# Kernel tuning notes

Hardware: AMD Instinct MI355X
Metric: run time of the kernel (lower is better)

## Reference

```python
import jax, jax.numpy as jnp
import numpy as np
from collections import defaultdict

H = 24; W = 24          # patch grid
B0 = 64                 # original batch (len(batch_id))
B = 128                 # total batch incl. augmented copies
C_IN = 256; HID = 128; HEADS_S = 2; OUT = 256; K = 9; NCLS = 8


def _build_space_edges():
    # knn_graph on the normalized meshgrid coords; identical for every image -> offset copies.
    P = H * W
    coords = np.stack(np.meshgrid(np.arange(H), np.arange(W), indexing='ij'), -1).reshape(-1, 2).astype(np.float32)
    cn = coords / coords.max()
    d = ((cn[:, None, :] - cn[None, :, :]) ** 2).sum(-1)
    np.fill_diagonal(d, np.inf)              # loop=False
    nbr = np.argsort(d, axis=1)[:, :K]       # [P, K] neighbor (source) ids
    off = (np.arange(B0) * P)[:, None, None]
    src = (nbr[None] + off).reshape(-1)
    dst = (np.broadcast_to(np.arange(P)[:, None], (P, K))[None] + off).reshape(-1)
    return np.stack([src, dst]).astype(np.int64)


def _build_view_edges(bid_all):
    groups = defaultdict(list)
    for i, c in enumerate(bid_all.tolist()):
        groups[c].append(i)
    ei = []
    for c, mem in groups.items():
        for a in range(len(mem)):
            for b in range(a + 1, len(mem)):
                i, j = mem[a], mem[b]
                if i >= B0 and j >= B0:
                    continue               # skip augmented-augmented pairs
                ei.append((i, j)); ei.append((j, i))
    return np.array(ei, dtype=np.int64).T


def setup_inputs() -> dict:
    key = jax.random.key(0)
    ks = jax.random.split(key, 8)
    bid = np.repeat(np.arange(NCLS), B0 // NCLS).astype(np.int64)
    bid_all = np.concatenate([bid, bid])
    s = 0.05
    return {
        'x': jax.random.normal(ks[0], (B, C_IN, H, W), jnp.float32),
        'batch_id_all': jnp.asarray(bid_all),
        'batch_id': jnp.asarray(bid),
        'edge_index_space': jnp.asarray(_build_space_edges()),
        'edge_index_view': jnp.asarray(_build_view_edges(bid_all)),
        'W_space': jax.random.normal(ks[1], (C_IN, HEADS_S * HID), jnp.float32) * s,
        'att_src_space': jax.random.normal(ks[2], (HEADS_S, HID), jnp.float32) * s,
        'att_dst_space': jax.random.normal(ks[3], (HEADS_S, HID), jnp.float32) * s,
        'bias_space': jnp.zeros((HEADS_S * HID,), jnp.float32),
        'W_view': jax.random.normal(ks[4], (HEADS_S * HID, OUT), jnp.float32) * s,
        'att_src_view': jax.random.normal(ks[5], (1, OUT), jnp.float32) * s,
        'att_dst_view': jax.random.normal(ks[6], (1, OUT), jnp.float32) * s,
        'bias_view': jnp.zeros((OUT,), jnp.float32),
    }


def _gat(xn, edges, Wm, a_src, a_dst, bias, heads, outc):
    # PyG GATConv: linear -> per-edge leaky_relu attn -> segment softmax over dst -> scatter-add
    N = xn.shape[0]
    loops = jnp.arange(N, dtype=edges.dtype)              # add_self_loops=True
    src = jnp.concatenate([edges[0], loops])
    dst = jnp.concatenate([edges[1], loops])
    h = (xn @ Wm).reshape(N, heads, outc)                 # [N, H, C]
    a_s = jnp.sum(h * a_src[None], -1)                    # [N, H]
    a_d = jnp.sum(h * a_dst[None], -1)
    e = jax.nn.leaky_relu(a_s[src] + a_d[dst], 0.2)       # [E, H]
    m = jax.ops.segment_max(e, dst, num_segments=N)
    ee = jnp.exp(e - m[dst])
    ssum = jax.ops.segment_sum(ee, dst, num_segments=N)
    alpha = ee / (ssum[dst] + 1e-16)
    out = jax.ops.segment_sum(h[src] * alpha[..., None], dst, num_segments=N)
    return out.reshape(N, heads * outc) + bias            # concat=True


def reference(x, batch_id_all, batch_id, edge_index_space, edge_index_view,
              W_space, att_src_space, att_dst_space, bias_space,
              W_view, att_src_view, att_dst_view, bias_view):
    P = H * W
    node = x[:B0].transpose(0, 2, 3, 1).reshape(-1, C_IN)                # [B0*P, C_in]
    x_space = _gat(node, edge_index_space, W_space, att_src_space,
                   att_dst_space, bias_space, HEADS_S, HID)              # [B0*P, 256]
    emb = x_space.reshape(B0, P, -1).mean(axis=1)                        # per-image mean pool
    emb_all = emb[jnp.arange(B) % B0]                                    # augmented i -> i % B0
    feat = _gat(emb_all, edge_index_view, W_view, att_src_view,
                att_dst_view, bias_view, 1, OUT)                         # [B, 256]
    C = feat.shape[1]
    x_view = 0.5 * x_space.reshape(B0, P, C) + 0.5 * feat[:B0][:, None, :]
    # torch does .reshape(-1, C).view(B, C, H, W): a raw row-major reinterpret
    return x_view.reshape(B0, C, H, W)
```

## Files before the change

kernel.cpp:

```cpp
#include <hip/hip_runtime.h>

#define PGRID 576
#define NB0   64
#define NBTOT 128
#define CIN   256
#define KNN   9
#define NNODE (NB0 * PGRID)

typedef __attribute__((ext_vector_type(8))) short short8;
typedef __attribute__((ext_vector_type(4))) float f32x4;

__device__ __forceinline__ float bf2f(unsigned short u) {
    union { unsigned int i; float f; } v; v.i = ((unsigned int)u) << 16; return v.f;
}
__device__ __forceinline__ unsigned short f2b(float f) {
    unsigned int u = __float_as_uint(f);
    return (unsigned short)((u + 0x7FFFu + ((u >> 16) & 1u)) >> 16);
}

__global__ __launch_bounds__(256) void prep_w(const float* __restrict__ W,
                                              unsigned short* __restrict__ Wt) {
    __shared__ float tile[64][65];
    const int c0 = blockIdx.x * 64, j0 = blockIdx.y * 64;
    const int t = threadIdx.x, lo = t % 64, hi = t / 64;
#pragma unroll
    for (int r = 0; r < 16; ++r)
        tile[r * 4 + hi][lo] = W[(size_t)(c0 + r * 4 + hi) * 256 + j0 + lo];
    __syncthreads();
#pragma unroll
    for (int r = 0; r < 16; ++r)
        Wt[(size_t)(j0 + r * 4 + hi) * 256 + c0 + lo] = f2b(tile[lo][r * 4 + hi]);
}

__global__ __launch_bounds__(256) void prep_x(const float* __restrict__ x,
                                              unsigned short* __restrict__ xbf) {
    __shared__ float tile[64][65];
    const int pt = blockIdx.x, ct = blockIdx.y, b = blockIdx.z;
    const int t = threadIdx.x, lo = t % 64, hi = t / 64;
    const float* xb = x + (size_t)b * CIN * PGRID;
#pragma unroll
    for (int r = 0; r < 16; ++r)
        tile[r * 4 + hi][lo] = xb[(size_t)(ct * 64 + r * 4 + hi) * PGRID + pt * 64 + lo];
    __syncthreads();
    const size_t nbase = (size_t)b * PGRID + pt * 64;
#pragma unroll
    for (int r = 0; r < 16; ++r)
        xbf[(nbase + r * 4 + hi) * 256 + ct * 64 + lo] = f2b(tile[lo][r * 4 + hi]);
}

__global__ __launch_bounds__(256) void gemm_mfma(const unsigned short* __restrict__ xbf,
                                                 const unsigned short* __restrict__ Wt,
                                                 unsigned short* __restrict__ h) {
    __shared__ char lds[65536];
    const int t  = threadIdx.x;
    const int n0 = blockIdx.x * 64;
    const int j0 = blockIdx.y * 64;
    const char* Ab = (const char*)xbf + (size_t)n0 * 512;
    const char* Bb = (const char*)Wt  + (size_t)j0 * 512;

#pragma unroll
    for (int pass = 0; pass < 8; ++pass) {
        const int p    = pass * 4096 + t * 16;
        const int row  = p >> 9;
        const int k16  = (p >> 4) & 31;
        const int src  = k16 ^ (row & 7);
        char* ldA = lds + pass * 4096 + (t & 192) * 16;
        char* ldB = ldA + 32768;
        __builtin_amdgcn_global_load_lds(Ab + (size_t)row * 512 + src * 16, ldA, 16, 0, 0);
        __builtin_amdgcn_global_load_lds(Bb + (size_t)row * 512 + src * 16, ldB, 16, 0, 0);
    }
    __syncthreads();

    const int l  = t & 63, w = t >> 6;
    const int qb = l >> 4;
    const int r7 = l & 7;
    const int rowA = w * 16 + (l & 15);
    const char* lA = lds + rowA * 512;
    f32x4 acc[4] = {};
#pragma unroll
    for (int ks = 0; ks < 8; ++ks) {
        const int q = (ks << 2) + qb;
        short8 a = *(const short8*)(lA + ((q ^ r7) << 4));
#pragma unroll
        for (int f = 0; f < 4; ++f) {
            short8 b = *(const short8*)(lds + 32768 + (f * 16 + (l & 15)) * 512 + ((q ^ r7) << 4));
            acc[f] = __builtin_amdgcn_mfma_f32_16x16x32_bf16(a, b, acc[f], 0, 0, 0);
        }
    }
    const int nb = n0 + w * 16 + ((l >> 4) << 2);
    const int jb = j0 + (l & 15);
#pragma unroll
    for (int f = 0; f < 4; ++f)
#pragma unroll
        for (int r = 0; r < 4; ++r)
            h[(size_t)(nb + r) * 256 + jb + f * 16] = f2b(acc[f][r]);
}

__global__ __launch_bounds__(256) void att_scores(const unsigned short* __restrict__ h,
                                                  const float* __restrict__ att_src,
                                                  const float* __restrict__ att_dst,
                                                  float* __restrict__ as_,
                                                  float* __restrict__ ad_) {
    const int wave = threadIdx.x >> 6;
    const int lane = threadIdx.x & 63;
    const int n = blockIdx.x * 4 + wave;
    const unsigned short* hr = h + (size_t)n * 256;
    float h0 = bf2f(hr[lane]), h1 = bf2f(hr[lane + 64]);
    float h2 = bf2f(hr[lane + 128]), h3 = bf2f(hr[lane + 192]);
    float s0 = h0 * att_src[lane]       + h1 * att_src[lane + 64];
    float s1 = h2 * att_src[lane + 128] + h3 * att_src[lane + 192];
    float d0 = h0 * att_dst[lane]       + h1 * att_dst[lane + 64];
    float d1 = h2 * att_dst[lane + 128] + h3 * att_dst[lane + 192];
#pragma unroll
    for (int off = 32; off > 0; off >>= 1) {
        s0 += __shfl_down(s0, off);
        s1 += __shfl_down(s1, off);
        d0 += __shfl_down(d0, off);
        d1 += __shfl_down(d1, off);
    }
    if (lane == 0) {
        as_[n * 2] = s0; as_[n * 2 + 1] = s1;
        ad_[n * 2] = d0; ad_[n * 2 + 1] = d1;
    }
}

__global__ __launch_bounds__(256) void space_gather(const unsigned short* __restrict__ h,
                                                    const float* __restrict__ as_,
                                                    const float* __restrict__ ad_,
                                                    const int* __restrict__ esrc,
                                                    const float* __restrict__ bias,
                                                    float* __restrict__ xs) {
    __shared__ int   s_src[10];
    __shared__ float s_e[10][2];
    const int n = blockIdx.x;
    const int t = threadIdx.x;
    if (t < 10) {
        int src = (t < 9) ? esrc[(size_t)n * KNN + t] : n;
        s_src[t] = src;
        float ad0 = ad_[n * 2], ad1 = ad_[n * 2 + 1];
        float e0 = as_[src * 2]     + ad0;
        float e1 = as_[src * 2 + 1] + ad1;
        s_e[t][0] = e0 >= 0.f ? e0 : 0.2f * e0;
        s_e[t][1] = e1 >= 0.f ? e1 : 0.2f * e1;
    }
    __syncthreads();
    const int head = t >> 7;
    float m = -1e30f;
#pragma unroll
    for (int k = 0; k < 10; ++k) m = fmaxf(m, s_e[k][head]);
    float wt[10];
    float ssum = 0.f;
#pragma unroll
    for (int k = 0; k < 10; ++k) { wt[k] = __expf(s_e[k][head] - m); ssum += wt[k]; }
    const float inv = 1.f / (ssum + 1e-16f);
    float out = 0.f;
#pragma unroll
    for (int k = 0; k < 10; ++k) out += wt[k] * bf2f(h[(size_t)s_src[k] * 256 + t]);
    xs[(size_t)n * 256 + t] = out * inv + bias[t];
}

__global__ __launch_bounds__(256) void pool_partial(const float* __restrict__ xs,
                                                    float* __restrict__ emb) {
    const int b = blockIdx.x, ch = blockIdx.y, j = threadIdx.x;
    const float* base = xs + ((size_t)b * PGRID + ch * 64) * 256 + j;
    float s = 0.f;
#pragma unroll 8
    for (int p = 0; p < 64; ++p) s += base[p * 256];
    atomicAdd(&emb[b * 256 + j], s);
}

__global__ __launch_bounds__(256) void view_linear(const float* __restrict__ emb,
                                                   const float* __restrict__ Wv,
                                                   const float* __restrict__ att_s,
                                                   const float* __restrict__ att_d,
                                                   float* __restrict__ hv,
                                                   float* __restrict__ asv,
                                                   float* __restrict__ adv) {
    __shared__ float er[256];
    __shared__ float red[2][256];
    const int i = blockIdx.x;
    const int j = threadIdx.x;
    er[j] = emb[(i % 64) * 256 + j] * (1.f / 576.f);
    __syncthreads();
    float acc = 0.f;
    for (int c = 0; c < 256; ++c) acc += er[c] * Wv[c * 256 + j];
    hv[(size_t)i * 256 + j] = acc;
    red[0][j] = acc * att_s[j];
    red[1][j] = acc * att_d[j];
    __syncthreads();
    for (int off = 128; off > 0; off >>= 1) {
        if (j < off) { red[0][j] += red[0][j + off]; red[1][j] += red[1][j + off]; }
        __syncthreads();
    }
    if (j == 0) { asv[i] = red[0][0]; adv[i] = red[1][0]; }
}

__global__ __launch_bounds__(256) void view_gather(const float* __restrict__ hv,
                                                   const float* __restrict__ asv,
                                                   const float* __restrict__ adv,
                                                   const int* __restrict__ ev,
                                                   int Ev,
                                                   const float* __restrict__ bias,
                                                   float* __restrict__ feat) {
    __shared__ int cnt;
    __shared__ int s_src[32];
    const int d = blockIdx.x;
    const int t = threadIdx.x;
    if (t == 0) cnt = 0;
    __syncthreads();
    for (int e = t; e < Ev; e += 256) {
        if (ev[Ev + e] == d) {
            int pos = atomicAdd(&cnt, 1);
            s_src[pos] = ev[e];
        }
    }
    __syncthreads();
    const int ns = cnt;
    const float adval = adv[d];
    float m = -1e30f;
    float ev_[16];
#pragma unroll 1
    for (int k = 0; k < ns; ++k) {
        float e = asv[s_src[k]] + adval;
        e = e >= 0.f ? e : 0.2f * e;
        ev_[k] = e;
        m = fmaxf(m, e);
    }
    float eself = asv[d] + adval;
    eself = eself >= 0.f ? eself : 0.2f * eself;
    m = fmaxf(m, eself);
    float ssum = 0.f;
#pragma unroll 1
    for (int k = 0; k < ns; ++k) { ev_[k] = __expf(ev_[k] - m); ssum += ev_[k]; }
    float wself = __expf(eself - m);
    ssum += wself;
    const float inv = 1.f / (ssum + 1e-16f);
    float out = 0.f;
#pragma unroll 1
    for (int k = 0; k < ns; ++k) out += ev_[k] * hv[(size_t)s_src[k] * 256 + t];
    out += wself * hv[(size_t)d * 256 + t];
    feat[d * 256 + t] = out * inv + bias[t];
}

__global__ __launch_bounds__(256) void combine(const float* __restrict__ xs,
                                               const float* __restrict__ feat,
                                               float* __restrict__ out, int ntot4) {
    int i = blockIdx.x * blockDim.x + threadIdx.x;
    if (i >= ntot4) return;
    size_t f = (size_t)i * 4;
    int b = (int)(f / (PGRID * 256));
    int j = (int)(f & 255);
    float4 a  = *(const float4*)(xs + f);
    float4 fb = *(const float4*)(feat + b * 256 + j);
    float4 o;
    o.x = 0.5f * (a.x + fb.x);
    o.y = 0.5f * (a.y + fb.y);
    o.z = 0.5f * (a.z + fb.z);
    o.w = 0.5f * (a.w + fb.w);
    *(float4*)(out + f) = o;
}

extern "C" void kernel_launch(void* const* d_in, const int* in_sizes, int n_in,
                              void* d_out, int out_size, void* d_ws, size_t ws_size,
                              hipStream_t stream) {
    const float* x        = (const float*)d_in[0];
    const int*   e_space  = (const int*)d_in[3];
    const int*   e_view   = (const int*)d_in[4];
    const float* W_space  = (const float*)d_in[5];
    const float* att_ss   = (const float*)d_in[6];
    const float* att_ds   = (const float*)d_in[7];
    const float* bias_s   = (const float*)d_in[8];
    const float* W_view   = (const float*)d_in[9];
    const float* att_sv   = (const float*)d_in[10];
    const float* att_dv   = (const float*)d_in[11];
    const float* bias_v   = (const float*)d_in[12];
    float* out = (float*)d_out;

    const int Ev = in_sizes[4] / 2;

    char* ws = (char*)d_ws;
    unsigned short* hbf = (unsigned short*)ws;
    unsigned short* xbf = (unsigned short*)(ws + 18874368);
    unsigned short* Wt  = (unsigned short*)(ws + 2 * 18874368);
    float* xs   = (float*)(ws + 2 * 18874368 + 131072);
    float* as_  = xs  + (size_t)NNODE * 256;
    float* ad_  = as_ + NNODE * 2;
    float* emb  = ad_ + NNODE * 2;
    float* hv   = emb + 64 * 256;
    float* asv  = hv  + 128 * 256;
    float* adv  = asv + 128;
    float* feat = adv + 128;

    prep_w<<<dim3(4, 4), 256, 0, stream>>>(W_space, Wt);
    prep_x<<<dim3(9, 4, 64), 256, 0, stream>>>(x, xbf);
    gemm_mfma<<<dim3(NNODE / 64, 4), 256, 0, stream>>>(xbf, Wt, hbf);
    att_scores<<<NNODE / 4, 256, 0, stream>>>(hbf, att_ss, att_ds, as_, ad_);
    space_gather<<<NNODE, 256, 0, stream>>>(hbf, as_, ad_, e_space, bias_s, xs);
    hipMemsetAsync(emb, 0, 64 * 256 * sizeof(float), stream);
    pool_partial<<<dim3(64, 9), 256, 0, stream>>>(xs, emb);
    view_linear<<<NBTOT, 256, 0, stream>>>(emb, W_view, att_sv, att_dv, hv, asv, adv);
    view_gather<<<NB0, 256, 0, stream>>>(hv, asv, adv, e_view, Ev, bias_v, feat);

    const int ntot4 = NB0 * PGRID * 256 / 4;
    combine<<<(ntot4 + 255) / 256, 256, 0, stream>>>(xs, feat, out, ntot4);
}
```

Before: 242.2 us.

## Fuse x transpose/convert and attention scores into a full-width MFMA GEMM

Removes the separate prep_x transpose pass and att_scores kernel. The GEMM now reads fp32 x directly in its channel-major layout, converts it to bf16 in registers, and computes all 256 output columns per block, so each wave computes attention dot products from its accumulators. The gather handles two nodes per block with vectorized bf16x2 loads. Pooling writes per-segment partial sums instead of using atomics and a memset. The cost is strided, uncoalesced global reads of x and a much larger register footprint (64 floats plus 16 accumulators), which may lower occupancy.

New measurement: 216.7 us. -10.5%, faster.

```diff
diff --git a/kernel.cpp b/kernel.cpp
--- a/kernel.cpp
+++ b/kernel.cpp
@@ -2,7 +2,6 @@
 
 #define PGRID 576
 #define NB0   64
-#define NBTOT 128
 #define CIN   256
 #define KNN   9
 #define NNODE (NB0 * PGRID)
@@ -32,144 +31,176 @@
         Wt[(size_t)(j0 + r * 4 + hi) * 256 + c0 + lo] = f2b(tile[lo][r * 4 + hi]);
 }
 
-__global__ __launch_bounds__(256) void prep_x(const float* __restrict__ x,
-                                              unsigned short* __restrict__ xbf) {
-    __shared__ float tile[64][65];
-    const int pt = blockIdx.x, ct = blockIdx.y, b = blockIdx.z;
-    const int t = threadIdx.x, lo = t % 64, hi = t / 64;
-    const float* xb = x + (size_t)b * CIN * PGRID;
-#pragma unroll
-    for (int r = 0; r < 16; ++r)
-        tile[r * 4 + hi][lo] = xb[(size_t)(ct * 64 + r * 4 + hi) * PGRID + pt * 64 + lo];
-    __syncthreads();
-    const size_t nbase = (size_t)b * PGRID + pt * 64;
-#pragma unroll
-    for (int r = 0; r < 16; ++r)
-        xbf[(nbase + r * 4 + hi) * 256 + ct * 64 + lo] = f2b(tile[lo][r * 4 + hi]);
-}
-
-__global__ __launch_bounds__(256) void gemm_mfma(const unsigned short* __restrict__ xbf,
-                                                 const unsigned short* __restrict__ Wt,
-                                                 unsigned short* __restrict__ h) {
-    __shared__ char lds[65536];
+__global__ __launch_bounds__(256) void gemm_fused(
+    const float* __restrict__ x, const unsigned short* __restrict__ Wt,
+    const float* __restrict__ att_src, const float* __restrict__ att_dst,
+    unsigned short* __restrict__ h, float* __restrict__ as_, float* __restrict__ ad_) {
+    __shared__ char ldsB[65536];
+    const int bx = blockIdx.x;
     const int t  = threadIdx.x;
-    const int n0 = blockIdx.x * 64;
-    const int j0 = blockIdx.y * 64;
-    const char* Ab = (const char*)xbf + (size_t)n0 * 512;
-    const char* Bb = (const char*)Wt  + (size_t)j0 * 512;
-
-#pragma unroll
-    for (int pass = 0; pass < 8; ++pass) {
-        const int p    = pass * 4096 + t * 16;
-        const int row  = p >> 9;
-        const int k16  = (p >> 4) & 31;
-        const int src  = k16 ^ (row & 7);
-        char* ldA = lds + pass * 4096 + (t & 192) * 16;
-        char* ldB = ldA + 32768;
-        __builtin_amdgcn_global_load_lds(Ab + (size_t)row * 512 + src * 16, ldA, 16, 0, 0);
-        __builtin_amdgcn_global_load_lds(Bb + (size_t)row * 512 + src * 16, ldB, 16, 0, 0);
-    }
-    __syncthreads();
-
-    const int l  = t & 63, w = t >> 6;
-    const int qb = l >> 4;
-    const int r7 = l & 7;
-    const int rowA = w * 16 + (l & 15);
-    const char* lA = lds + rowA * 512;
-    f32x4 acc[4] = {};
-#pragma unroll
-    for (int ks = 0; ks < 8; ++ks) {
-        const int q = (ks << 2) + qb;
-        short8 a = *(const short8*)(lA + ((q ^ r7) << 4));
-#pragma unroll
-        for (int f = 0; f < 4; ++f) {
-            short8 b = *(const short8*)(lds + 32768 + (f * 16 + (l & 15)) * 512 + ((q ^ r7) << 4));
-            acc[f] = __builtin_amdgcn_mfma_f32_16x16x32_bf16(a, b, acc[f], 0, 0, 0);
-        }
-    }
-    const int nb = n0 + w * 16 + ((l >> 4) << 2);
-    const int jb = j0 + (l & 15);
-#pragma unroll
-    for (int f = 0; f < 4; ++f)
+    const int b  = bx / 9;
+    const int p0 = (bx % 9) * 64;
+    const int n0 = bx * 64;
+    const int l = t & 63, w = t >> 6;
+    const int l4 = l >> 4, l15 = l & 15;
+    const float* xb = x + (size_t)b * (CIN * PGRID);
+
+    {
+        const int jrow = t >> 4, g = t & 15;
+#pragma unroll
+        for (int i = 0; i < 16; ++i) {
+            int j  = i * 16 + jrow;
+            int gs = (g & 8) | ((g & 7) ^ (j & 7));
+            __builtin_amdgcn_global_load_lds(
+                (const char*)Wt + (size_t)j * 512 + gs * 16,
+                ldsB + i * 4096 + (t & 192) * 16, 16, 0, 0);
+        }
+    }
+    const int prow = p0 + w * 16 + l15;
+    float a0[64];
+#pragma unroll
+    for (int ch = 0; ch < 2; ++ch)
+#pragma unroll
+        for (int q = 0; q < 4; ++q)
+#pragma unroll
+            for (int jj = 0; jj < 8; ++jj) {
+                int c = ch * 128 + q * 32 + l4 * 8 + jj;
+                a0[ch * 32 + q * 8 + jj] = xb[(size_t)c * PGRID + prow];
+            }
+    short8 apk[8];
+#pragma unroll
+    for (int cq = 0; cq < 8; ++cq) {
+        short8 v;
+#pragma unroll
+        for (int jj = 0; jj < 8; ++jj) v[jj] = (short)f2b(a0[cq * 8 + jj]);
+        apk[cq] = v;
+    }
+    f32x4 acc[16] = {};
+    __syncthreads();
+#pragma unroll
+    for (int q = 0; q < 4; ++q) {
+        const int gr = q * 4 + l4;
+#pragma unroll
+        for (int f = 0; f < 16; ++f) {
+            int j  = f * 16 + l15;
+            int gp = (gr & 8) | ((gr & 7) ^ (j & 7));
+            short8 bf = *(const short8*)(ldsB + j * 256 + gp * 16);
+            acc[f] = __builtin_amdgcn_mfma_f32_16x16x32_bf16(apk[q], bf, acc[f], 0, 0, 0);
+        }
+    }
+    __syncthreads();
+    {
+        const int jrow = t >> 4, g = t & 15;
+#pragma unroll
+        for (int i = 0; i < 16; ++i) {
+            int j  = i * 16 + jrow;
+            int gs = (g & 8) | ((g & 7) ^ (j & 7));
+            __builtin_amdgcn_global_load_lds(
+                (const char*)Wt + (size_t)j * 512 + 256 + gs * 16,
+                ldsB + i * 4096 + (t & 192) * 16, 16, 0, 0);
+        }
+    }
+    __syncthreads();
+#pragma unroll
+    for (int q = 0; q < 4; ++q) {
+        const int gr = q * 4 + l4;
+#pragma unroll
+        for (int f = 0; f < 16; ++f) {
+            int j  = f * 16 + l15;
+            int gp = (gr & 8) | ((gr & 7) ^ (j & 7));
+            short8 bf = *(const short8*)(ldsB + j * 256 + gp * 16);
+            acc[f] = __builtin_amdgcn_mfma_f32_16x16x32_bf16(apk[4 + q], bf, acc[f], 0, 0, 0);
+        }
+    }
+    const int nb = n0 + w * 16 + l4 * 4;
+#pragma unroll
+    for (int f = 0; f < 16; ++f)
 #pragma unroll
         for (int r = 0; r < 4; ++r)
-            h[(size_t)(nb + r) * 256 + jb + f * 16] = f2b(acc[f][r]);
-}
-
-__global__ __launch_bounds__(256) void att_scores(const unsigned short* __restrict__ h,
-                                                  const float* __restrict__ att_src,
-                                                  const float* __restrict__ att_dst,
-                                                  float* __restrict__ as_,
-                                                  float* __restrict__ ad_) {
-    const int wave = threadIdx.x >> 6;
-    const int lane = threadIdx.x & 63;
-    const int n = blockIdx.x * 4 + wave;
-    const unsigned short* hr = h + (size_t)n * 256;
-    float h0 = bf2f(hr[lane]), h1 = bf2f(hr[lane + 64]);
-    float h2 = bf2f(hr[lane + 128]), h3 = bf2f(hr[lane + 192]);
-    float s0 = h0 * att_src[lane]       + h1 * att_src[lane + 64];
-    float s1 = h2 * att_src[lane + 128] + h3 * att_src[lane + 192];
-    float d0 = h0 * att_dst[lane]       + h1 * att_dst[lane + 64];
-    float d1 = h2 * att_dst[lane + 128] + h3 * att_dst[lane + 192];
-#pragma unroll
-    for (int off = 32; off > 0; off >>= 1) {
-        s0 += __shfl_down(s0, off);
-        s1 += __shfl_down(s1, off);
-        d0 += __shfl_down(d0, off);
-        d1 += __shfl_down(d1, off);
-    }
-    if (lane == 0) {
-        as_[n * 2] = s0; as_[n * 2 + 1] = s1;
-        ad_[n * 2] = d0; ad_[n * 2 + 1] = d1;
-    }
-}
-
-__global__ __launch_bounds__(256) void space_gather(const unsigned short* __restrict__ h,
-                                                    const float* __restrict__ as_,
-                                                    const float* __restrict__ ad_,
-                                                    const int* __restrict__ esrc,
-                                                    const float* __restrict__ bias,
-                                                    float* __restrict__ xs) {
-    __shared__ int   s_src[10];
-    __shared__ float s_e[10][2];
-    const int n = blockIdx.x;
+            h[(size_t)(nb + r) * 256 + l15 + f * 16] = f2b(acc[f][r]);
+
+    float av[16], dvv[16];
+#pragma unroll
+    for (int f = 0; f < 16; ++f) {
+        av[f]  = att_src[f * 16 + l15];
+        dvv[f] = att_dst[f * 16 + l15];
+    }
+#pragma unroll
+    for (int r = 0; r < 4; ++r) {
+        float s0 = 0.f, s1 = 0.f, d0 = 0.f, d1 = 0.f;
+#pragma unroll
+        for (int f = 0; f < 8; ++f)  { s0 += acc[f][r] * av[f];  d0 += acc[f][r] * dvv[f]; }
+#pragma unroll
+        for (int f = 8; f < 16; ++f) { s1 += acc[f][r] * av[f];  d1 += acc[f][r] * dvv[f]; }
+#pragma unroll
+        for (int m = 1; m < 16; m <<= 1) {
+            s0 += __shfl_xor(s0, m); s1 += __shfl_xor(s1, m);
+            d0 += __shfl_xor(d0, m); d1 += __shfl_xor(d1, m);
+        }
+        if (l15 == 0) {
+            int n = nb + r;
+            as_[n * 2] = s0; as_[n * 2 + 1] = s1;
+            ad_[n * 2] = d0; ad_[n * 2 + 1] = d1;
+        }
+    }
+}
+
+__global__ __launch_bounds__(256) void space_gather(
+    const unsigned short* __restrict__ h, const float* __restrict__ as_,
+    const float* __restrict__ ad_, const int* __restrict__ esrc,
+    const float* __restrict__ bias, float* __restrict__ xs) {
+    __shared__ int   s_src[2][10];
+    __shared__ float s_e[2][10][2];
     const int t = threadIdx.x;
-    if (t < 10) {
-        int src = (t < 9) ? esrc[(size_t)n * KNN + t] : n;
-        s_src[t] = src;
-        float ad0 = ad_[n * 2], ad1 = ad_[n * 2 + 1];
-        float e0 = as_[src * 2]     + ad0;
-        float e1 = as_[src * 2 + 1] + ad1;
-        s_e[t][0] = e0 >= 0.f ? e0 : 0.2f * e0;
-        s_e[t][1] = e1 >= 0.f ? e1 : 0.2f * e1;
-    }
-    __syncthreads();
-    const int head = t >> 7;
+    const int node = t >> 7;
+    const int idx  = t & 127;
+    const int n = blockIdx.x * 2 + node;
+    if (idx < 10) {
+        int src = (idx < 9) ? esrc[(size_t)n * KNN + idx] : n;
+        s_src[node][idx] = src;
+        float e0 = as_[src * 2]     + ad_[n * 2];
+        float e1 = as_[src * 2 + 1] + ad_[n * 2 + 1];
+        s_e[node][idx][0] = e0 >= 0.f ? e0 : 0.2f * e0;
+        s_e[node][idx][1] = e1 >= 0.f ? e1 : 0.2f * e1;
+    }
+    __syncthreads();
+    const int j2 = idx * 2;
+    const int head = idx >> 6;
     float m = -1e30f;
 #pragma unroll
-    for (int k = 0; k < 10; ++k) m = fmaxf(m, s_e[k][head]);
-    float wt[10];
-    float ssum = 0.f;
-#pragma unroll
-    for (int k = 0; k < 10; ++k) { wt[k] = __expf(s_e[k][head] - m); ssum += wt[k]; }
+    for (int k = 0; k < 10; ++k) m = fmaxf(m, s_e[node][k][head]);
+    float wgt[10]; float ssum = 0.f;
+#pragma unroll
+    for (int k = 0; k < 10; ++k) { wgt[k] = __expf(s_e[node][k][head] - m); ssum += wgt[k]; }
     const float inv = 1.f / (ssum + 1e-16f);
-    float out = 0.f;
-#pragma unroll
-    for (int k = 0; k < 10; ++k) out += wt[k] * bf2f(h[(size_t)s_src[k] * 256 + t]);
-    xs[(size_t)n * 256 + t] = out * inv + bias[t];
+    float o0 = 0.f, o1 = 0.f;
+#pragma unroll
+    for (int k = 0; k < 10; ++k) {
+        unsigned int v = *(const unsigned int*)(h + (size_t)s_src[node][k] * 256 + j2);
+        o0 += wgt[k] * bf2f((unsigned short)(v & 0xffff));
+        o1 += wgt[k] * bf2f((unsigned short)(v >> 16));
+    }
+    float2 res;
+    res.x = o0 * inv + bias[j2];
+    res.y = o1 * inv + bias[j2 + 1];
+    *(float2*)(xs + (size_t)n * 256 + j2) = res;
 }
 
 __global__ __launch_bounds__(256) void pool_partial(const float* __restrict__ xs,
-                                                    float* __restrict__ emb) {
-    const int b = blockIdx.x, ch = blockIdx.y, j = threadIdx.x;
-    const float* base = xs + ((size_t)b * PGRID + ch * 64) * 256 + j;
-    float s = 0.f;
-#pragma unroll 8
-    for (int p = 0; p < 64; ++p) s += base[p * 256];
-    atomicAdd(&emb[b * 256 + j], s);
-}
-
-__global__ __launch_bounds__(256) void view_linear(const float* __restrict__ emb,
+                                                    float* __restrict__ embp) {
+    const int b   = blockIdx.x;
+    const int f4  = threadIdx.x & 63;
+    const int seg = threadIdx.x >> 6;
+    const float* base = xs + ((size_t)b * PGRID + seg * 144) * 256 + f4 * 4;
+    float4 s = {0.f, 0.f, 0.f, 0.f};
+    for (int p = 0; p < 144; ++p) {
+        float4 v = *(const float4*)(base + (size_t)p * 256);
+        s.x += v.x; s.y += v.y; s.z += v.z; s.w += v.w;
+    }
+    *(float4*)(embp + ((size_t)b * 4 + seg) * 256 + f4 * 4) = s;
+}
+
+__global__ __launch_bounds__(256) void view_linear(const float* __restrict__ embp,
                                                    const float* __restrict__ Wv,
                                                    const float* __restrict__ att_s,
                                                    const float* __restrict__ att_d,
@@ -180,7 +211,10 @@
     __shared__ float red[2][256];
     const int i = blockIdx.x;
     const int j = threadIdx.x;
-    er[j] = emb[(i % 64) * 256 + j] * (1.f / 576.f);
+    const int i64 = i & 63;
+    er[j] = (embp[((size_t)i64 * 4 + 0) * 256 + j] + embp[((size_t)i64 * 4 + 1) * 256 + j] +
+             embp[((size_t)i64 * 4 + 2) * 256 + j] + embp[((size_t)i64 * 4 + 3) * 256 + j]) *
+            (1.f / 576.f);
     __syncthreads();
     float acc = 0.f;
     for (int c = 0; c < 256; ++c) acc += er[c] * Wv[c * 256 + j];
@@ -280,25 +314,21 @@
 
     char* ws = (char*)d_ws;
     unsigned short* hbf = (unsigned short*)ws;
-    unsigned short* xbf = (unsigned short*)(ws + 18874368);
-    unsigned short* Wt  = (unsigned short*)(ws + 2 * 18874368);
-    float* xs   = (float*)(ws + 2 * 18874368 + 131072);
+    unsigned short* Wt  = (unsigned short*)(ws + 18874368);
+    float* xs   = (float*)(ws + 18874368 + 131072);
     float* as_  = xs  + (size_t)NNODE * 256;
     float* ad_  = as_ + NNODE * 2;
-    float* emb  = ad_ + NNODE * 2;
-    float* hv   = emb + 64 * 256;
+    float* embp = ad_ + NNODE * 2;
+    float* hv   = embp + 64 * 4 * 256;
     float* asv  = hv  + 128 * 256;
     float* adv  = asv + 128;
     float* feat = adv + 128;
 
     prep_w<<<dim3(4, 4), 256, 0, stream>>>(W_space, Wt);
-    prep_x<<<dim3(9, 4, 64), 256, 0, stream>>>(x, xbf);
-    gemm_mfma<<<dim3(NNODE / 64, 4), 256, 0, stream>>>(xbf, Wt, hbf);
-    att_scores<<<NNODE / 4, 256, 0, stream>>>(hbf, att_ss, att_ds, as_, ad_);
-    space_gather<<<NNODE, 256, 0, stream>>>(hbf, as_, ad_, e_space, bias_s, xs);
-    hipMemsetAsync(emb, 0, 64 * 256 * sizeof(float), stream);
-    pool_partial<<<dim3(64, 9), 256, 0, stream>>>(xs, emb);
-    view_linear<<<NBTOT, 256, 0, stream>>>(emb, W_view, att_sv, att_dv, hv, asv, adv);
+    gemm_fused<<<576, 256, 0, stream>>>(x, Wt, att_ss, att_ds, hbf, as_, ad_);
+    space_gather<<<NNODE / 2, 256, 0, stream>>>(hbf, as_, ad_, e_space, bias_s, xs);
+    pool_partial<<<NB0, 256, 0, stream>>>(xs, embp);
+    view_linear<<<128, 256, 0, stream>>>(embp, W_view, att_sv, att_dv, hv, asv, adv);
     view_gather<<<NB0, 256, 0, stream>>>(hv, asv, adv, e_view, Ev, bias_v, feat);
 
     const int ntot4 = NB0 * PGRID * 256 / 4;
```
